# Optimization experiments

Measured on AMD Instinct MI355X. Metric: run time of the kernel, lower is better.

Reference implementation:

```python
import jax, jax.numpy as jnp
import numpy as np

NUM_HEADS = 12


def setup_inputs() -> dict:
    key = jax.random.key(0)
    k1, k2, k3 = jax.random.split(key, 3)
    B, N, D = 8, 1024, 768
    x = jax.random.normal(k1, (B, N, D), dtype=jnp.float32)
    Wqkv = jax.random.normal(k2, (D, 3 * D), dtype=jnp.float32) * (D ** -0.5)
    Wproj = jax.random.normal(k3, (D, D), dtype=jnp.float32) * (D ** -0.5)
    bproj = jnp.zeros((D,), dtype=jnp.float32)
    return {"x": x, "Wqkv": Wqkv, "Wproj": Wproj, "bproj": bproj}


def reference(x, Wqkv, Wproj, bproj):
    B, N, D = x.shape
    H = NUM_HEADS
    d = D // H
    scale = d ** -0.5
    qkv = x @ Wqkv  # [B, N, 3D]; qkv_bias=False
    # 'b n (qkv h d) -> qkv b h n d'
    qkv = qkv.reshape(B, N, 3, H, d)
    q = jnp.transpose(qkv[:, :, 0], (0, 2, 1, 3))  # [B, H, N, d]
    k = jnp.transpose(qkv[:, :, 1], (0, 2, 1, 3))
    v = jnp.transpose(qkv[:, :, 2], (0, 2, 1, 3))
    attn = jnp.einsum('bhnd,bhmd->bhnm', q, k) * scale  # [B, H, N, N]
    attn = jax.nn.softmax(attn, axis=-1)
    out = jnp.einsum('bhnm,bhmd->bhnd', attn, v)  # [B, H, N, d]
    out = jnp.transpose(out, (0, 2, 1, 3)).reshape(B, N, D)  # 'b h n d -> b n (h d)'
    return out @ Wproj + bproj
```

## Files before the change

kernel.cpp:

```cpp
#include <hip/hip_runtime.h>
#include <math.h>
#include <stdint.h>

namespace {

constexpr int Nseq = 1024;
constexpr int Dm = 768;
constexpr int threeD = 2304;
constexpr int Mrows = 8192;
constexpr int Hh = 12;
constexpr float kScaleLog2 = 0.18033688011112042f;

using bf16x8 = __attribute__((ext_vector_type(8))) short;
using f32x4 = __attribute__((ext_vector_type(4))) float;
using f32x16 = __attribute__((ext_vector_type(16))) float;
using us4 = __attribute__((ext_vector_type(4))) unsigned short;

__device__ __forceinline__ unsigned short f2bf(float f) {
  union { float f; uint32_t u; } v;
  v.f = f;
  uint32_t r = v.u + 0x7fffu + ((v.u >> 16) & 1u);
  return (unsigned short)(r >> 16);
}

__device__ __forceinline__ float fexp2(float x) {
#if __has_builtin(__builtin_amdgcn_exp2f)
  return __builtin_amdgcn_exp2f(x);
#else
  float r;
  asm("v_exp_f32 %0, %1\n\ts_nop 0" : "=v"(r) : "v"(x));
  return r;
#endif
}

__device__ __forceinline__ uint32_t cvtpk_bf16(float lo, float hi) {
  uint32_t r;
  asm("v_cvt_pk_bf16_f32 %0, %1, %2" : "=v"(r) : "v"(lo), "v"(hi));
  return r;
}

__device__ __forceinline__ void gload_lds16(const void* g, void* l) {
  __builtin_amdgcn_global_load_lds(
      (const __attribute__((address_space(1))) unsigned int*)(uintptr_t)g,
      (__attribute__((address_space(3))) unsigned int*)(uintptr_t)l, 16, 0, 0);
}

__global__ __launch_bounds__(256) void cast_f32_bf16(
    const float* __restrict__ in, unsigned short* __restrict__ outp, int n4) {
  int i = blockIdx.x * blockDim.x + threadIdx.x;
  if (i < n4) {
    float4 v = ((const float4*)in)[i];
    us4 u = {f2bf(v.x), f2bf(v.y), f2bf(v.z), f2bf(v.w)};
    ((us4*)outp)[i] = u;
  }
}

__global__ __launch_bounds__(256) void transpose_cast(
    const float* __restrict__ W, unsigned short* __restrict__ Wt, int K, int N) {
  __shared__ unsigned short tile[32][33];
  const int n0 = blockIdx.x * 32, k0 = blockIdx.y * 32;
  const int tx = threadIdx.x & 31, ty = threadIdx.x >> 5;
#pragma unroll
  for (int i = 0; i < 32; i += 8)
    tile[ty + i][tx] = f2bf(W[(size_t)(k0 + ty + i) * N + n0 + tx]);
  __syncthreads();
#pragma unroll
  for (int i = 0; i < 32; i += 8)
    Wt[(size_t)(n0 + ty + i) * K + k0 + tx] = tile[tx][ty + i];
}

template <int MODE, int BM, int NCOLS>
__global__ __launch_bounds__(256) void gemm_bf16(
    const unsigned short* __restrict__ A, const unsigned short* __restrict__ Bt,
    void* __restrict__ C0, void* __restrict__ C1,
    const float* __restrict__ bias, int K) {
  constexpr int ASL = BM * 4;
  constexpr int TS = ASL + 512;
  constexpr int LPS = TS / 256;
  constexpr int MF = BM / 32;
  __shared__ unsigned short As[3][ASL * 8];
  __shared__ unsigned short Bs[3][512 * 8];
  const int tid = threadIdx.x;
  const int wid = tid >> 6;
  const int lane = tid & 63;
  const int l15 = lane & 15, lg = lane >> 4;
  const int p = blockIdx.x;
  const int cpx = gridDim.x >> 3;
  const int l = (p & 7) * cpx + (p >> 3);
  const int row0 = (l / NCOLS) * BM, col0 = (l % NCOLS) * 128;
  const int wr = (wid >> 1) * (BM / 2), wc = (wid & 1) * 64;

  auto stage = [&](int k0, int bufi) {
    unsigned short* as = As[bufi];
    unsigned short* bs = Bs[bufi];
#pragma unroll
    for (int it = 0; it < LPS; ++it) {
      const int s = it * 256 + tid;
      if (s < ASL) {
        const int r = s >> 2, c = s & 3;
        const int g = c ^ ((r >> 1) & 3);
        gload_lds16(&A[(size_t)(row0 + r) * K + k0 + g * 8],
                    &as[(s & ~63) * 8]);
      } else {
        const int s2 = s - ASL;
        const int r = s2 >> 2, c = s2 & 3;
        const int g = c ^ ((r >> 1) & 3);
        gload_lds16(&Bt[(size_t)(col0 + r) * K + k0 + g * 8],
                    &bs[(s2 & ~63) * 8]);
      }
    }
  };

  f32x4 acc[MF][4] = {};
  const int nt = K / 32;
  stage(0, 0);
  stage(32, 1);
  for (int t = 0; t < nt; ++t) {
    const int cur = t % 3;
    if (t + 2 < nt) {
      stage((t + 2) * 32, (t + 2) % 3);
      asm volatile("s_waitcnt vmcnt(%0)" ::"i"(2 * LPS) : "memory");
    } else if (t + 1 < nt) {
      asm volatile("s_waitcnt vmcnt(%0)" ::"i"(LPS) : "memory");
    } else {
      asm volatile("s_waitcnt vmcnt(0)" ::: "memory");
    }
    __builtin_amdgcn_s_barrier();
    bf16x8 av[MF], bv[4];
#pragma unroll
    for (int m = 0; m < MF; ++m) {
      const int ar = wr + m * 16 + l15;
      av[m] = *(const bf16x8*)&As[cur][(ar * 4 + (lg ^ ((ar >> 1) & 3))) * 8];
    }
#pragma unroll
    for (int n = 0; n < 4; ++n) {
      const int br = wc + n * 16 + l15;
      bv[n] = *(const bf16x8*)&Bs[cur][(br * 4 + (lg ^ ((br >> 1) & 3))) * 8];
    }
#pragma unroll
    for (int m = 0; m < MF; ++m)
#pragma unroll
      for (int n = 0; n < 4; ++n)
        acc[m][n] =
            __builtin_amdgcn_mfma_f32_16x16x32_bf16(av[m], bv[n], acc[m][n], 0, 0, 0);
    asm volatile("s_waitcnt lgkmcnt(0)" ::: "memory");
    __builtin_amdgcn_sched_barrier(0);
    __builtin_amdgcn_s_barrier();
  }
  if constexpr (MODE == 1) {
#pragma unroll
    for (int m = 0; m < MF; ++m)
#pragma unroll
      for (int n = 0; n < 4; ++n) {
        const int col = col0 + wc + n * 16 + l15;
#pragma unroll
        for (int rr = 0; rr < 4; ++rr)
          ((float*)C0)[(size_t)(row0 + wr + m * 16 + lg * 4 + rr) * Dm + col] =
              acc[m][n][rr] + bias[col];
      }
  } else if (col0 < 1536) {
#pragma unroll
    for (int m = 0; m < MF; ++m)
#pragma unroll
      for (int n = 0; n < 4; ++n) {
        const int col = col0 + wc + n * 16 + l15;
        const float qs = (col < 768) ? kScaleLog2 : 1.f;
#pragma unroll
        for (int rr = 0; rr < 4; ++rr)
          ((unsigned short*)C0)[(size_t)(row0 + wr + m * 16 + lg * 4 + rr) * 1536 +
                                col] = f2bf(acc[m][n][rr] * qs);
      }
  } else {
#pragma unroll
    for (int m = 0; m < MF; ++m)
#pragma unroll
      for (int n = 0; n < 4; ++n) {
        const int c = col0 + wc + n * 16 + l15 - 1536;
        const int row = row0 + wr + m * 16 + lg * 4;
        const int bb = row >> 10, n0 = row & 1023;
        us4 pk = {f2bf(acc[m][n][0]), f2bf(acc[m][n][1]), f2bf(acc[m][n][2]),
                  f2bf(acc[m][n][3])};
        *(us4*)&((unsigned short*)C1)[((size_t)bb * 768 + c) * 1024 + n0] = pk;
      }
  }
}

__global__ __launch_bounds__(256) void attn_mfma(
    const unsigned short* __restrict__ qkb, const unsigned short* __restrict__ vtb,
    unsigned short* __restrict__ outb) {
  constexpr int NT = Nseq / 64;
  __shared__ unsigned short Ks[2][64 * 64];
  __shared__ unsigned short Vs[2][64 * 64];
  const int tid = threadIdx.x;
  const int wid = tid >> 6, lane = tid & 63;
  const int l31 = lane & 31, hi = lane >> 5;
  const int p = blockIdx.x;
  const int l = (p & 7) * 96 + (p >> 3);
  const int qt = l & 7;
  const int hb = l >> 3;
  const int h = hb % Hh, b = hb / Hh;
  const size_t rb = (size_t)b * Nseq;
  const int hoff = h * 64;
  const size_t vbase = ((size_t)b * 768 + hoff) * 1024;

  const int qrow = qt * 128 + wid * 32 + l31;
  bf16x8 Qf[4];
#pragma unroll
  for (int ks = 0; ks < 4; ++ks)
    Qf[ks] = *(const bf16x8*)&qkb[(rb + qrow) * 1536 + hoff + ks * 16 + hi * 8];

  int strow[2], scol[2];
#pragma unroll
  for (int it = 0; it < 2; ++it) {
    const int ci = it * 256 + wid * 64 + lane;
    const int tr = ci >> 3, cc = ci & 7;
    strow[it] = tr;
    scol[it] = (cc ^ (tr & 7)) * 8;
  }

  auto stage = [&](int kt, int bufi) {
#pragma unroll
    for (int it = 0; it < 2; ++it) {
      const int ldsoff = (it * 256 + wid * 64) * 8;
      gload_lds16(&qkb[(rb + kt * 64 + strow[it]) * 1536 + 768 + hoff + scol[it]],
                  &Ks[bufi][ldsoff]);
      gload_lds16(&vtb[vbase + (size_t)strow[it] * 1024 + kt * 64 + scol[it]],
                  &Vs[bufi][ldsoff]);
    }
  };

  float l_run = 0.f;
  f32x16 o0 = {}, o1 = {};

  stage(0, 0);

  for (int kt = 0; kt < NT; ++kt) {
    const int bufi = kt & 1;
    if (kt + 1 < NT) {
      stage(kt + 1, bufi ^ 1);
      asm volatile("s_waitcnt vmcnt(4)" ::: "memory");
    } else {
      asm volatile("s_waitcnt vmcnt(0)" ::: "memory");
    }
    __builtin_amdgcn_s_barrier();
    const unsigned short* ksb = Ks[bufi];
    const unsigned short* vsb = Vs[bufi];
    f32x16 s0 = {}, s1 = {};
    __builtin_amdgcn_s_setprio(1);
#pragma unroll
    for (int ks = 0; ks < 4; ++ks) {
      const int c = 2 * ks + hi;
      {
        const int tr = l31;
        bf16x8 kf = *(const bf16x8*)&ksb[tr * 64 + ((c ^ (tr & 7)) * 8)];
        s0 = __builtin_amdgcn_mfma_f32_32x32x16_bf16(kf, Qf[ks], s0, 0, 0, 0);
      }
      {
        const int tr = l31 + 32;
        bf16x8 kf = *(const bf16x8*)&ksb[tr * 64 + ((c ^ (tr & 7)) * 8)];
        s1 = __builtin_amdgcn_mfma_f32_32x32x16_bf16(kf, Qf[ks], s1, 0, 0, 0);
      }
    }
    __builtin_amdgcn_s_setprio(0);
#pragma unroll
    for (int i = 0; i < 16; ++i) {
      s0[i] = fexp2(s0[i]);
      s1[i] = fexp2(s1[i]);
    }
    float a[8];
#pragma unroll
    for (int i = 0; i < 8; ++i)
      a[i] = (s0[i] + s0[i + 8]) + (s1[i] + s1[i + 8]);
#pragma unroll
    for (int st = 4; st >= 1; st >>= 1)
#pragma unroll
      for (int i = 0; i < st; ++i) a[i] += a[i + st];
    l_run += a[0];
    bf16x8 Pf[4];
#pragma unroll
    for (int ks = 0; ks < 4; ++ks) {
      const f32x16 sv = (ks >> 1) ? s1 : s0;
      const int e0 = 8 * (ks & 1);
      uint32_t pe01 = cvtpk_bf16(sv[e0 + 0], sv[e0 + 1]);
      uint32_t pe23 = cvtpk_bf16(sv[e0 + 2], sv[e0 + 3]);
      uint32_t po01 = cvtpk_bf16(sv[e0 + 4], sv[e0 + 5]);
      uint32_t po23 = cvtpk_bf16(sv[e0 + 6], sv[e0 + 7]);
      asm("v_permlane32_swap_b32 %0, %1" : "+v"(pe01), "+v"(po01));
      asm("v_permlane32_swap_b32 %0, %1" : "+v"(pe23), "+v"(po23));
      union {
        uint32_t w[4];
        bf16x8 v;
      } u;
      u.w[0] = pe01;
      u.w[1] = pe23;
      u.w[2] = po01;
      u.w[3] = po23;
      Pf[ks] = u.v;
    }
    __builtin_amdgcn_s_setprio(1);
#pragma unroll
    for (int ks = 0; ks < 4; ++ks) {
      const int c = 2 * ks + hi;
      {
        const int tr = l31;
        bf16x8 vf = *(const bf16x8*)&vsb[tr * 64 + ((c ^ (tr & 7)) * 8)];
        o0 = __builtin_amdgcn_mfma_f32_32x32x16_bf16(vf, Pf[ks], o0, 0, 0, 0);
      }
      {
        const int tr = l31 + 32;
        bf16x8 vf = *(const bf16x8*)&vsb[tr * 64 + ((c ^ (tr & 7)) * 8)];
        o1 = __builtin_amdgcn_mfma_f32_32x32x16_bf16(vf, Pf[ks], o1, 0, 0, 0);
      }
    }
    __builtin_amdgcn_s_setprio(0);
    asm volatile("s_waitcnt lgkmcnt(0)" ::: "memory");
    __builtin_amdgcn_sched_barrier(0);
    __builtin_amdgcn_s_barrier();
  }
  const float lsum = l_run + __shfl_xor(l_run, 32);
  const float linv = 1.f / lsum;
  const size_t obase = (size_t)(rb + qrow) * Dm + hoff;
#pragma unroll
  for (int g = 0; g < 4; ++g) {
    us4 a4 = {f2bf(o0[g * 4 + 0] * linv), f2bf(o0[g * 4 + 1] * linv),
              f2bf(o0[g * 4 + 2] * linv), f2bf(o0[g * 4 + 3] * linv)};
    *(us4*)&outb[obase + g * 8 + hi * 4] = a4;
    us4 b4 = {f2bf(o1[g * 4 + 0] * linv), f2bf(o1[g * 4 + 1] * linv),
              f2bf(o1[g * 4 + 2] * linv), f2bf(o1[g * 4 + 3] * linv)};
    *(us4*)&outb[obase + 32 + g * 8 + hi * 4] = b4;
  }
}

}

extern "C" void kernel_launch(void* const* d_in, const int* in_sizes, int n_in,
                              void* d_out, int out_size, void* d_ws,
                              size_t ws_size, hipStream_t stream) {
  (void)in_sizes;
  (void)n_in;
  (void)out_size;
  (void)ws_size;
  const float* x = (const float*)d_in[0];
  const float* Wqkv = (const float*)d_in[1];
  const float* Wproj = (const float*)d_in[2];
  const float* bproj = (const float*)d_in[3];
  float* out = (float*)d_out;

  char* w = (char*)d_ws;
  unsigned short* xb = (unsigned short*)w;
  w += (size_t)Mrows * Dm * 2;
  unsigned short* wqkvt = (unsigned short*)w;
  w += (size_t)threeD * Dm * 2;
  unsigned short* wprojt = (unsigned short*)w;
  w += (size_t)Dm * Dm * 2;
  unsigned short* qkb = (unsigned short*)w;
  w += (size_t)Mrows * 1536 * 2;
  unsigned short* vtb = (unsigned short*)w;
  w += (size_t)96 * 64 * 1024 * 2;
  unsigned short* attnb = (unsigned short*)w;

  cast_f32_bf16<<<(Mrows * Dm / 4 + 255) / 256, 256, 0, stream>>>(
      x, xb, Mrows * Dm / 4);
  transpose_cast<<<dim3(threeD / 32, Dm / 32), 256, 0, stream>>>(
      Wqkv, wqkvt, Dm, threeD);
  transpose_cast<<<dim3(Dm / 32, Dm / 32), 256, 0, stream>>>(Wproj, wprojt, Dm, Dm);
  gemm_bf16<0, 128, 18><<<dim3(1152), 256, 0, stream>>>(
      xb, wqkvt, qkb, vtb, nullptr, Dm);
  attn_mfma<<<dim3(768), 256, 0, stream>>>(qkb, vtb, attnb);
  gemm_bf16<1, 64, 6><<<dim3(768), 256, 0, stream>>>(
      attnb, wprojt, out, nullptr, bproj, Dm);
}
```

Before: 121.3 us.

## Replace GEMMs with 8-wave 128x256 tile kernel with interleaved prefetch

Replaces the 4-wave triple-buffered GEMM with an 8-wave, 128x256-tile, K=64 double-buffered kernel. Global-to-LDS prefetch of the next tile is split into two halves interleaved between MFMA phases, and s_setprio is raised around the MFMA blocks. The aim is more data reuse per tile, fewer loop iterations and better overlap of loads with compute. The output projection now launches only 192 blocks, which is fewer than the CU count and may leave compute units idle.

```diff
diff --git a/kernel.cpp b/kernel.cpp
--- a/kernel.cpp
+++ b/kernel.cpp
@@ -69,87 +69,120 @@
     Wt[(size_t)(n0 + ty + i) * K + k0 + tx] = tile[tx][ty + i];
 }
 
-template <int MODE, int BM, int NCOLS>
-__global__ __launch_bounds__(256) void gemm_bf16(
+template <int MODE, int NCOLS>
+__global__ __launch_bounds__(512) void gemm8(
     const unsigned short* __restrict__ A, const unsigned short* __restrict__ Bt,
     void* __restrict__ C0, void* __restrict__ C1,
-    const float* __restrict__ bias, int K) {
-  constexpr int ASL = BM * 4;
-  constexpr int TS = ASL + 512;
-  constexpr int LPS = TS / 256;
-  constexpr int MF = BM / 32;
-  __shared__ unsigned short As[3][ASL * 8];
-  __shared__ unsigned short Bs[3][512 * 8];
+    const float* __restrict__ bias, int Kdim) {
+  __shared__ unsigned short As[2][128 * 64];
+  __shared__ unsigned short Bs[2][256 * 64];
   const int tid = threadIdx.x;
-  const int wid = tid >> 6;
-  const int lane = tid & 63;
+  const int wid = tid >> 6, lane = tid & 63;
   const int l15 = lane & 15, lg = lane >> 4;
   const int p = blockIdx.x;
   const int cpx = gridDim.x >> 3;
   const int l = (p & 7) * cpx + (p >> 3);
-  const int row0 = (l / NCOLS) * BM, col0 = (l % NCOLS) * 128;
-  const int wr = (wid >> 1) * (BM / 2), wc = (wid & 1) * 64;
-
-  auto stage = [&](int k0, int bufi) {
-    unsigned short* as = As[bufi];
-    unsigned short* bs = Bs[bufi];
-#pragma unroll
-    for (int it = 0; it < LPS; ++it) {
-      const int s = it * 256 + tid;
-      if (s < ASL) {
-        const int r = s >> 2, c = s & 3;
-        const int g = c ^ ((r >> 1) & 3);
-        gload_lds16(&A[(size_t)(row0 + r) * K + k0 + g * 8],
-                    &as[(s & ~63) * 8]);
-      } else {
-        const int s2 = s - ASL;
-        const int r = s2 >> 2, c = s2 & 3;
-        const int g = c ^ ((r >> 1) & 3);
-        gload_lds16(&Bt[(size_t)(col0 + r) * K + k0 + g * 8],
-                    &bs[(s2 & ~63) * 8]);
-      }
-    }
+  const int row0 = (l / NCOLS) * 128, col0 = (l % NCOLS) * 256;
+  const int wr = (wid >> 2) * 64, wc = (wid & 3) * 64;
+
+  auto stageA = [&](int kt, int b, int r) {
+    const int s = r * 512 + tid;
+    const int row = s >> 3, c = s & 7;
+    const int sc = c ^ (row & 7);
+    gload_lds16(&A[(size_t)(row0 + row) * Kdim + kt * 64 + sc * 8],
+                &As[b][(s & ~63) * 8]);
   };
-
-  f32x4 acc[MF][4] = {};
-  const int nt = K / 32;
-  stage(0, 0);
-  stage(32, 1);
-  for (int t = 0; t < nt; ++t) {
-    const int cur = t % 3;
-    if (t + 2 < nt) {
-      stage((t + 2) * 32, (t + 2) % 3);
-      asm volatile("s_waitcnt vmcnt(%0)" ::"i"(2 * LPS) : "memory");
-    } else if (t + 1 < nt) {
-      asm volatile("s_waitcnt vmcnt(%0)" ::"i"(LPS) : "memory");
-    } else {
-      asm volatile("s_waitcnt vmcnt(0)" ::: "memory");
-    }
-    __builtin_amdgcn_s_barrier();
-    bf16x8 av[MF], bv[4];
-#pragma unroll
-    for (int m = 0; m < MF; ++m) {
-      const int ar = wr + m * 16 + l15;
-      av[m] = *(const bf16x8*)&As[cur][(ar * 4 + (lg ^ ((ar >> 1) & 3))) * 8];
-    }
-#pragma unroll
-    for (int n = 0; n < 4; ++n) {
-      const int br = wc + n * 16 + l15;
-      bv[n] = *(const bf16x8*)&Bs[cur][(br * 4 + (lg ^ ((br >> 1) & 3))) * 8];
-    }
-#pragma unroll
-    for (int m = 0; m < MF; ++m)
-#pragma unroll
-      for (int n = 0; n < 4; ++n)
-        acc[m][n] =
-            __builtin_amdgcn_mfma_f32_16x16x32_bf16(av[m], bv[n], acc[m][n], 0, 0, 0);
+  auto stageB = [&](int kt, int b, int r) {
+    const int s = r * 512 + tid;
+    const int row = s >> 3, c = s & 7;
+    const int sc = c ^ (row & 7);
+    gload_lds16(&Bt[(size_t)(col0 + row) * Kdim + kt * 64 + sc * 8],
+                &Bs[b][(s & ~63) * 8]);
+  };
+  auto rdA = [&](int b, int m, int ks) {
+    const int row = wr + m * 16 + l15;
+    const int sc = (ks * 4 + lg) ^ (row & 7);
+    return *(const bf16x8*)&As[b][(row * 8 + sc) * 8];
+  };
+  auto rdB = [&](int b, int n, int ks) {
+    const int row = wc + n * 16 + l15;
+    const int sc = (ks * 4 + lg) ^ (row & 7);
+    return *(const bf16x8*)&Bs[b][(row * 8 + sc) * 8];
+  };
+
+  f32x4 acc[4][4] = {};
+  stageA(0, 0, 0);
+  stageA(0, 0, 1);
+  stageB(0, 0, 0);
+  stageB(0, 0, 1);
+  stageB(0, 0, 2);
+  stageB(0, 0, 3);
+  asm volatile("s_waitcnt vmcnt(0)" ::: "memory");
+  __builtin_amdgcn_s_barrier();
+
+  const int NTK = Kdim / 64;
+  for (int g = 0; g < NTK; ++g) {
+    const int cur = g & 1;
+    const int nb = cur ^ 1;
+    const bool pf = (g + 1 < NTK);
+    bf16x8 bfr[4][2], afr[2][2];
+#pragma unroll
+    for (int n = 0; n < 4; ++n)
+#pragma unroll
+      for (int ks = 0; ks < 2; ++ks) bfr[n][ks] = rdB(cur, n, ks);
+#pragma unroll
+    for (int m = 0; m < 2; ++m)
+#pragma unroll
+      for (int ks = 0; ks < 2; ++ks) afr[m][ks] = rdA(cur, m, ks);
+    if (pf) {
+      stageA(g + 1, nb, 0);
+      stageA(g + 1, nb, 1);
+      stageB(g + 1, nb, 0);
+    }
+    __builtin_amdgcn_s_barrier();
     asm volatile("s_waitcnt lgkmcnt(0)" ::: "memory");
     __builtin_amdgcn_sched_barrier(0);
-    __builtin_amdgcn_s_barrier();
-  }
+    __builtin_amdgcn_s_setprio(1);
+#pragma unroll
+    for (int m = 0; m < 2; ++m)
+#pragma unroll
+      for (int n = 0; n < 4; ++n)
+#pragma unroll
+        for (int ks = 0; ks < 2; ++ks)
+          acc[m][n] = __builtin_amdgcn_mfma_f32_16x16x32_bf16(
+              afr[m][ks], bfr[n][ks], acc[m][n], 0, 0, 0);
+    __builtin_amdgcn_s_setprio(0);
+    __builtin_amdgcn_s_barrier();
+#pragma unroll
+    for (int m = 0; m < 2; ++m)
+#pragma unroll
+      for (int ks = 0; ks < 2; ++ks) afr[m][ks] = rdA(cur, m + 2, ks);
+    if (pf) {
+      stageB(g + 1, nb, 1);
+      stageB(g + 1, nb, 2);
+      stageB(g + 1, nb, 3);
+    }
+    __builtin_amdgcn_s_barrier();
+    asm volatile("s_waitcnt lgkmcnt(0)" ::: "memory");
+    __builtin_amdgcn_sched_barrier(0);
+    __builtin_amdgcn_s_setprio(1);
+#pragma unroll
+    for (int m = 0; m < 2; ++m)
+#pragma unroll
+      for (int n = 0; n < 4; ++n)
+#pragma unroll
+        for (int ks = 0; ks < 2; ++ks)
+          acc[m + 2][n] = __builtin_amdgcn_mfma_f32_16x16x32_bf16(
+              afr[m][ks], bfr[n][ks], acc[m + 2][n], 0, 0, 0);
+    __builtin_amdgcn_s_setprio(0);
+    asm volatile("s_waitcnt vmcnt(0)" ::: "memory");
+    __builtin_amdgcn_sched_barrier(0);
+    __builtin_amdgcn_s_barrier();
+  }
+
   if constexpr (MODE == 1) {
 #pragma unroll
-    for (int m = 0; m < MF; ++m)
+    for (int m = 0; m < 4; ++m)
 #pragma unroll
       for (int n = 0; n < 4; ++n) {
         const int col = col0 + wc + n * 16 + l15;
@@ -158,30 +191,32 @@
           ((float*)C0)[(size_t)(row0 + wr + m * 16 + lg * 4 + rr) * Dm + col] =
               acc[m][n][rr] + bias[col];
       }
-  } else if (col0 < 1536) {
-#pragma unroll
-    for (int m = 0; m < MF; ++m)
-#pragma unroll
-      for (int n = 0; n < 4; ++n) {
-        const int col = col0 + wc + n * 16 + l15;
-        const float qs = (col < 768) ? kScaleLog2 : 1.f;
-#pragma unroll
-        for (int rr = 0; rr < 4; ++rr)
-          ((unsigned short*)C0)[(size_t)(row0 + wr + m * 16 + lg * 4 + rr) * 1536 +
-                                col] = f2bf(acc[m][n][rr] * qs);
-      }
   } else {
-#pragma unroll
-    for (int m = 0; m < MF; ++m)
-#pragma unroll
-      for (int n = 0; n < 4; ++n) {
-        const int c = col0 + wc + n * 16 + l15 - 1536;
-        const int row = row0 + wr + m * 16 + lg * 4;
-        const int bb = row >> 10, n0 = row & 1023;
-        us4 pk = {f2bf(acc[m][n][0]), f2bf(acc[m][n][1]), f2bf(acc[m][n][2]),
-                  f2bf(acc[m][n][3])};
-        *(us4*)&((unsigned short*)C1)[((size_t)bb * 768 + c) * 1024 + n0] = pk;
-      }
+    if (col0 < 1536) {
+#pragma unroll
+      for (int m = 0; m < 4; ++m)
+#pragma unroll
+        for (int n = 0; n < 4; ++n) {
+          const int col = col0 + wc + n * 16 + l15;
+          const float qs = (col < 768) ? kScaleLog2 : 1.f;
+#pragma unroll
+          for (int rr = 0; rr < 4; ++rr)
+            ((unsigned short*)C0)[(size_t)(row0 + wr + m * 16 + lg * 4 + rr) *
+                                      1536 + col] = f2bf(acc[m][n][rr] * qs);
+        }
+    } else {
+#pragma unroll
+      for (int m = 0; m < 4; ++m)
+#pragma unroll
+        for (int n = 0; n < 4; ++n) {
+          const int c = col0 + wc + n * 16 + l15 - 1536;
+          const int row = row0 + wr + m * 16 + lg * 4;
+          const int bb = row >> 10, n0 = row & 1023;
+          us4 pk = {f2bf(acc[m][n][0]), f2bf(acc[m][n][1]), f2bf(acc[m][n][2]),
+                    f2bf(acc[m][n][3])};
+          *(us4*)&((unsigned short*)C1)[((size_t)bb * 768 + c) * 1024 + n0] = pk;
+        }
+    }
   }
 }
 
@@ -364,9 +399,8 @@
   transpose_cast<<<dim3(threeD / 32, Dm / 32), 256, 0, stream>>>(
       Wqkv, wqkvt, Dm, threeD);
   transpose_cast<<<dim3(Dm / 32, Dm / 32), 256, 0, stream>>>(Wproj, wprojt, Dm, Dm);
-  gemm_bf16<0, 128, 18><<<dim3(1152), 256, 0, stream>>>(
-      xb, wqkvt, qkb, vtb, nullptr, Dm);
+  gemm8<0, 9><<<dim3(576), 512, 0, stream>>>(xb, wqkvt, qkb, vtb, nullptr, Dm);
   attn_mfma<<<dim3(768), 256, 0, stream>>>(qkb, vtb, attnb);
-  gemm_bf16<1, 64, 6><<<dim3(768), 256, 0, stream>>>(
-      attnb, wprojt, out, nullptr, bproj, Dm);
-}
+  gemm8<1, 3><<<dim3(192), 512, 0, stream>>>(attnb, wprojt, out, nullptr, bproj,
+                                             Dm);
+}
```

New measurement: 125.1 us. 1.03x slower.

## Software-pipeline attention: triple-buffer K/V and overlap next QK with current softmax-PV

Applied to the files above, without the earlier changes.

Converts the attention loop to a three-stage LDS ring buffer that prefetches two tiles ahead. It computes the QK scores for tile t+1 before doing the exp, bf16 pack and PV MFMA for tile t, so the MFMA and exp/VALU work of consecutive tiles can interleave. This costs extra LDS (three K/V buffers instead of two) and a second set of score accumulator registers, which may lower occupancy or raise register pressure.

```diff
diff --git a/kernel.cpp b/kernel.cpp
--- a/kernel.cpp
+++ b/kernel.cpp
@@ -189,8 +189,8 @@
     const unsigned short* __restrict__ qkb, const unsigned short* __restrict__ vtb,
     unsigned short* __restrict__ outb) {
   constexpr int NT = Nseq / 64;
-  __shared__ unsigned short Ks[2][64 * 64];
-  __shared__ unsigned short Vs[2][64 * 64];
+  __shared__ unsigned short Ks[3][64 * 64];
+  __shared__ unsigned short Vs[3][64 * 64];
   const int tid = threadIdx.x;
   const int wid = tid >> 6, lane = tid & 63;
   const int l31 = lane & 31, hi = lane >> 5;
@@ -232,20 +232,10 @@
   float l_run = 0.f;
   f32x16 o0 = {}, o1 = {};
 
-  stage(0, 0);
-
-  for (int kt = 0; kt < NT; ++kt) {
-    const int bufi = kt & 1;
-    if (kt + 1 < NT) {
-      stage(kt + 1, bufi ^ 1);
-      asm volatile("s_waitcnt vmcnt(4)" ::: "memory");
-    } else {
-      asm volatile("s_waitcnt vmcnt(0)" ::: "memory");
-    }
-    __builtin_amdgcn_s_barrier();
-    const unsigned short* ksb = Ks[bufi];
-    const unsigned short* vsb = Vs[bufi];
-    f32x16 s0 = {}, s1 = {};
+  auto qk = [&](int bidx, f32x16& d0, f32x16& d1) {
+    const unsigned short* ksb = Ks[bidx];
+    d0 = {};
+    d1 = {};
     __builtin_amdgcn_s_setprio(1);
 #pragma unroll
     for (int ks = 0; ks < 4; ++ks) {
@@ -253,15 +243,18 @@
       {
         const int tr = l31;
         bf16x8 kf = *(const bf16x8*)&ksb[tr * 64 + ((c ^ (tr & 7)) * 8)];
-        s0 = __builtin_amdgcn_mfma_f32_32x32x16_bf16(kf, Qf[ks], s0, 0, 0, 0);
+        d0 = __builtin_amdgcn_mfma_f32_32x32x16_bf16(kf, Qf[ks], d0, 0, 0, 0);
       }
       {
         const int tr = l31 + 32;
         bf16x8 kf = *(const bf16x8*)&ksb[tr * 64 + ((c ^ (tr & 7)) * 8)];
-        s1 = __builtin_amdgcn_mfma_f32_32x32x16_bf16(kf, Qf[ks], s1, 0, 0, 0);
+        d1 = __builtin_amdgcn_mfma_f32_32x32x16_bf16(kf, Qf[ks], d1, 0, 0, 0);
       }
     }
     __builtin_amdgcn_s_setprio(0);
+  };
+
+  auto finish = [&](int bidx, f32x16& s0, f32x16& s1) {
 #pragma unroll
     for (int i = 0; i < 16; ++i) {
       s0[i] = fexp2(s0[i]);
@@ -297,6 +290,7 @@
       u.w[3] = po23;
       Pf[ks] = u.v;
     }
+    const unsigned short* vsb = Vs[bidx];
     __builtin_amdgcn_s_setprio(1);
 #pragma unroll
     for (int ks = 0; ks < 4; ++ks) {
@@ -313,9 +307,32 @@
       }
     }
     __builtin_amdgcn_s_setprio(0);
+  };
+
+  auto step = [&](int t, f32x16& c0, f32x16& c1, f32x16& n0, f32x16& n1) {
+    if (t + 2 < NT) {
+      stage(t + 2, (t + 2) % 3);
+      asm volatile("s_waitcnt vmcnt(4)" ::: "memory");
+    } else {
+      asm volatile("s_waitcnt vmcnt(0)" ::: "memory");
+    }
+    __builtin_amdgcn_s_barrier();
+    if (t + 1 < NT) qk((t + 1) % 3, n0, n1);
+    finish(t % 3, c0, c1);
     asm volatile("s_waitcnt lgkmcnt(0)" ::: "memory");
     __builtin_amdgcn_sched_barrier(0);
     __builtin_amdgcn_s_barrier();
+  };
+
+  stage(0, 0);
+  stage(1, 1);
+  asm volatile("s_waitcnt vmcnt(4)" ::: "memory");
+  __builtin_amdgcn_s_barrier();
+  f32x16 sA0, sA1, sB0, sB1;
+  qk(0, sA0, sA1);
+  for (int t = 0; t < NT; t += 2) {
+    step(t, sA0, sA1, sB0, sB1);
+    step(t + 1, sB0, sB1, sA0, sA1);
   }
   const float lsum = l_run + __shfl_xor(l_run, 32);
   const float linv = 1.f / lsum;
```

New measurement: 120.1 us. Within noise of the previous version (-0.9%).
